# Performance work log

Hardware: AMD Instinct MI355X
Metric: run time of the kernel (lower is better)

Reference implementation:

```python
import jax, jax.numpy as jnp
import numpy as np

B, L, C = 2, 2048, 1024
DK, H = 64, 16

def setup_inputs() -> dict:
    key = jax.random.key(0)
    ks = jax.random.split(key, 12)
    def lin(kw, kb, out_dim, in_dim):
        w = jax.random.normal(kw, (out_dim, in_dim), jnp.float32) * (1.0 / np.sqrt(in_dim))
        b = jnp.zeros((out_dim,), jnp.float32)
        return w, b
    WQ_w, WQ_b = lin(ks[0], ks[1], DK * H, C)
    WK_w, WK_b = lin(ks[2], ks[3], DK * H, C)
    WV_w, WV_b = lin(ks[4], ks[5], DK * H, C)
    WO_w, WO_b = lin(ks[6], ks[7], C, DK * H)
    qx = jax.random.normal(ks[8], (B, L, C), jnp.float32)
    kx = jax.random.normal(ks[9], (B, L, C), jnp.float32)
    vx = jax.random.normal(ks[10], (B, L, C), jnp.float32)
    maskPAD = jax.random.randint(ks[11], (B, L, L), 0, 2, jnp.int32)
    return {"qx": qx, "kx": kx, "vx": vx, "maskPAD": maskPAD,
            "WQ_w": WQ_w, "WQ_b": WQ_b, "WK_w": WK_w, "WK_b": WK_b,
            "WV_w": WV_w, "WV_b": WV_b, "WO_w": WO_w, "WO_b": WO_b}

def reference(qx, kx, vx, maskPAD, WQ_w, WQ_b, WK_w, WK_b, WV_w, WV_b, WO_w, WO_b):
    Bq, qL, _ = qx.shape
    kvL = kx.shape[1]
    # projections -> [B, H, L, DK]
    q = (qx @ WQ_w.T + WQ_b).reshape(Bq, qL, H, DK).transpose(0, 2, 1, 3)
    k = (kx @ WK_w.T + WK_b).reshape(Bq, kvL, H, DK).transpose(0, 2, 1, 3)
    v = (vx @ WV_w.T + WV_b).reshape(Bq, kvL, H, DK).transpose(0, 2, 1, 3)
    scores = jnp.einsum('bhqd,bhkd->bhqk', q, k) / np.sqrt(DK).astype(np.float32)
    scores = jnp.where((maskPAD == 0)[:, None, :, :], jnp.float32(-2**15 + 1), scores)
    alpha = jax.nn.softmax(scores, axis=3)  # dropout p=0 (eval)
    z = jnp.einsum('bhqk,bhkd->bhqd', alpha, v)
    z = z.transpose(0, 2, 1, 3).reshape(Bq, qL, H * DK)
    return z @ WO_w.T + WO_b
```

## Files before the change

### kernel.cpp

```cpp
#include <hip/hip_runtime.h>
#include <hip/hip_bf16.h>
#include <stdint.h>
#include <math.h>

typedef short short8 __attribute__((ext_vector_type(8)));
typedef short short4v __attribute__((ext_vector_type(4)));
typedef float float4v __attribute__((ext_vector_type(4)));
typedef float float2v __attribute__((ext_vector_type(2)));

static __device__ __forceinline__ float bf2f(uint16_t u) {
    union { uint32_t i; float f; } x; x.i = ((uint32_t)u) << 16; return x.f;
}
static __device__ __forceinline__ uint16_t f2bf(float f) {
    union { float f; uint32_t i; } x; x.f = f;
    uint32_t u = x.i;
    u += 0x7FFFu + ((u >> 16) & 1u);
    return (uint16_t)(u >> 16);
}
static __device__ __forceinline__ uint16_t f2bf_hw(float f) {
    __hip_bfloat16 h = __float2bfloat16(f);
    uint16_t u; __builtin_memcpy(&u, &h, 2); return u;
}
static __device__ __forceinline__ uint16_t f2bf_sane(float f) {
    uint16_t u = f2bf(f);
    if ((u & 0x7F80u) == 0x7F80u) u = 0;
    return u;
}
static __device__ __forceinline__ float san_f32(float f) {
    union { float f; uint32_t i; } x; x.f = f;
    if (((x.i >> 23) & 0xFFu) == 0xFFu) return 0.f;
    return x.f;
}
static __device__ __forceinline__ void gll16(const void* g, void* l) {
    __builtin_amdgcn_global_load_lds((const __attribute__((address_space(1))) void*)g,
                                     (__attribute__((address_space(3))) void*)l,
                                     16, 0, 0);
}
static __device__ __forceinline__ short8 load8(const void* p, size_t off, int fp32) {
    if (!fp32) return *(const short8*)((const uint16_t*)p + off);
    const float* f = (const float*)p + off;
    const float4v a = *(const float4v*)f;
    const float4v b = *(const float4v*)(f + 4);
    short8 r;
    r[0] = (short)f2bf(a[0]); r[1] = (short)f2bf(a[1]);
    r[2] = (short)f2bf(a[2]); r[3] = (short)f2bf(a[3]);
    r[4] = (short)f2bf(b[0]); r[5] = (short)f2bf(b[1]);
    r[6] = (short)f2bf(b[2]); r[7] = (short)f2bf(b[3]);
    return r;
}

static __device__ __forceinline__ float fexp2(float x) {
#if __has_builtin(__builtin_amdgcn_exp2f)
    return __builtin_amdgcn_exp2f(x);
#else
    float r; asm("v_exp_f32 %0, %1\ns_nop 0" : "=v"(r) : "v"(x)); return r;
#endif
}

static __device__ __forceinline__ float maskexp2(float s, uint32_t nib, int r) {
    union { float f; uint32_t u; } x; x.f = s;
    const uint32_t keep = (uint32_t)(((int32_t)(nib << (31 - r))) >> 31);
    x.u = (x.u & keep) | (~keep & 0xFF800000u);
    return fexp2(x.f);
}

static __device__ __forceinline__ float4v mfma16_bf16(short4v a, short4v b, float4v c) {
#if __has_builtin(__builtin_amdgcn_mfma_f32_16x16x16bf16_1k)
    return __builtin_amdgcn_mfma_f32_16x16x16bf16_1k(a, b, c, 0, 0, 0);
#else
    float4v d = c;
    asm volatile("v_mfma_f32_16x16x16_bf16 %0, %1, %2, %0"
                 : "+v"(d) : "v"(a), "v"(b));
    return d;
#endif
}

__global__ __launch_bounds__(256) void pack_kernel(
    const int* __restrict__ mask, uint64_t* __restrict__ mask64,
    const uint16_t* __restrict__ qx, int* __restrict__ flag)
{
    const int wave = threadIdx.x >> 6, lane = threadIdx.x & 63;
    if (blockIdx.x == 1024) {
        __shared__ int s;
        const int tid = threadIdx.x;
        if (tid == 0) s = 0;
        __syncthreads();
        int bad = 0;
#pragma unroll 8
        for (int i = 0; i < 64; ++i) {
            const uint16_t u = qx[tid * 64 + i];
            bad |= ((u & 0x7F80u) == 0x7F80u) ? 1 : 0;
        }
        if (bad) atomicOr(&s, 1);
        __syncthreads();
        if (tid == 0) *flag = s;
        return;
    }
    const int row = blockIdx.x * 4 + wave;
    const int* src = mask + (size_t)row * 2048;
#pragma unroll 4
    for (int j = 0; j < 32; ++j) {
        const int m = src[j * 64 + lane];
        const uint64_t bal = __ballot(m != 0);
        if (lane == 0) mask64[(size_t)row * 32 + j] = bal;
    }
}

__global__ __launch_bounds__(256) void convert_kernel(
    const void* qx, const void* kx, const void* vx,
    const void* wq, const void* wk, const void* wv, const void* wo,
    const void* bq, const void* bk, const void* bv, const void* bo,
    uint16_t* cIn, uint16_t* cW, uint16_t* cB, const int* flag)
{
    const int mode = *flag;
    if (!mode) return;
    const int z = blockIdx.z;
    if (z < 3) {
        const void* src = (z == 0) ? qx : (z == 1) ? kx : vx;
        uint16_t* dst = cIn + (size_t)z * 4194304;
#pragma unroll
        for (int it = 0; it < 8; ++it) {
            const int idx8 = (blockIdx.x * 8 + it) * 256 + threadIdx.x;
            *(short8*)(dst + (size_t)idx8 * 8) = load8(src, (size_t)idx8 * 8, 1);
        }
    } else if (z < 7) {
        const int t = z - 3;
        const void* src = (t == 0) ? wq : (t == 1) ? wk : (t == 2) ? wv : wo;
        uint16_t* dst = cW + (size_t)t * 1048576;
#pragma unroll
        for (int it = 0; it < 2; ++it) {
            const int idx8 = (blockIdx.x * 2 + it) * 256 + threadIdx.x;
            *(short8*)(dst + (size_t)idx8 * 8) = load8(src, (size_t)idx8 * 8, 1);
        }
    } else {
        const int idx8 = blockIdx.x * 256 + threadIdx.x;
        if (idx8 < 128) {
#pragma unroll
            for (int t = 0; t < 4; ++t) {
                const void* src = (t == 0) ? bq : (t == 1) ? bk : (t == 2) ? bv : bo;
                *(short8*)(cB + t * 1024 + idx8 * 8) = load8(src, (size_t)idx8 * 8, 1);
            }
        }
    }
}

template <int MI, int NI>
static __device__ __forceinline__ void gemm_tile(
    const uint16_t* __restrict__ A, const uint16_t* __restrict__ W,
    const uint16_t* __restrict__ bias, void* __restrict__ C,
    int c_fp32, float out_scale, int bx, int by)
{
    constexpr int TM = MI * 32, TN = NI * 32;
    __shared__ __align__(16) uint16_t sA[TM * 32];
    __shared__ __align__(16) uint16_t sB[TN * 32];

    const int tid  = threadIdx.x;
    const int wave = tid >> 6;
    const int lane = tid & 63;
    const int quad = lane >> 4;
    const int l15  = lane & 15;
    const int m0 = by * TM;
    const int n0 = bx * TN;
    const int wm = (wave >> 1) * (MI * 16);
    const int wn = (wave & 1) * (NI * 16);
    const int r16 = lane >> 2;
    const int ch  = lane & 3;

    float4v acc[MI][NI] = {};

    for (int k0 = 0; k0 < 1024; k0 += 32) {
        __syncthreads();
#pragma unroll
        for (int g = wave; g < TM / 16; g += 4)
            gll16(A + (size_t)(m0 + g * 16 + r16) * 1024 + k0 + ch * 8,
                  (char*)sA + (size_t)g * 1024);
#pragma unroll
        for (int g = wave; g < TN / 16; g += 4)
            gll16(W + (size_t)(n0 + g * 16 + r16) * 1024 + k0 + ch * 8,
                  (char*)sB + (size_t)g * 1024);
        asm volatile("s_waitcnt vmcnt(0)" ::: "memory");
        __syncthreads();

        short8 af[MI], bfr[NI];
#pragma unroll
        for (int i = 0; i < MI; ++i)
            af[i] = *(const short8*)&sA[(wm + i * 16 + l15) * 32 + quad * 8];
#pragma unroll
        for (int j = 0; j < NI; ++j)
            bfr[j] = *(const short8*)&sB[(wn + j * 16 + l15) * 32 + quad * 8];
#pragma unroll
        for (int mi = 0; mi < MI; ++mi)
#pragma unroll
            for (int ni = 0; ni < NI; ++ni)
                acc[mi][ni] = __builtin_amdgcn_mfma_f32_16x16x32_bf16(
                    af[mi], bfr[ni], acc[mi][ni], 0, 0, 0);
    }

#pragma unroll
    for (int ni = 0; ni < NI; ++ni) {
        const int n = n0 + wn + ni * 16 + l15;
        const float bv = bf2f(bias[n]);
#pragma unroll
        for (int mi = 0; mi < MI; ++mi) {
            const int mbase = m0 + wm + mi * 16 + quad * 4;
#pragma unroll
            for (int r = 0; r < 4; ++r) {
                const float v = (acc[mi][ni][r] + bv) * out_scale;
                const size_t idx = (size_t)(mbase + r) * 1024 + n;
                if (c_fp32) ((float*)C)[idx] = san_f32(v);
                else        ((uint16_t*)C)[idx] = f2bf_sane(v);
            }
        }
    }
}

__global__ __launch_bounds__(256) void qkv_kernel(
    const uint16_t* rqx, const uint16_t* rkx, const uint16_t* rvx,
    const uint16_t* rwq, const uint16_t* rwk, const uint16_t* rwv,
    const uint16_t* rbq, const uint16_t* rbk, const uint16_t* rbv,
    const uint16_t* cIn, const uint16_t* cW, const uint16_t* cB,
    uint16_t* Q, uint16_t* K, uint16_t* V, const int* flag)
{
    const int mode = *flag;
    const int wgid = blockIdx.x + (blockIdx.y << 3) + (blockIdx.z << 8);
    const int xcd = wgid & 7;
    const int s   = wgid >> 3;
    const int panel = xcd * 12 + (s >> 3);
    const int bx = s & 7;
    const int z  = panel >> 5;
    const int by = panel & 31;

    const uint16_t* A = mode ? cIn + (size_t)z * 4194304
                             : ((z == 0) ? rqx : (z == 1) ? rkx : rvx);
    const uint16_t* W = mode ? cW + (size_t)z * 1048576
                             : ((z == 0) ? rwq : (z == 1) ? rwk : rwv);
    const uint16_t* b = mode ? cB + z * 1024
                             : ((z == 0) ? rbq : (z == 1) ? rbk : rbv);
    uint16_t* C = (z == 0) ? Q : (z == 1) ? K : V;
    const float sc = (z == 0) ? 0.18033688f : 1.0f;
    gemm_tile<4, 4>(A, W, b, C, 0, sc, bx, by);
}

__global__ __launch_bounds__(256) void out_kernel(
    const uint16_t* Z, const uint16_t* rwo, const uint16_t* rbo,
    const uint16_t* cW, const uint16_t* cB, void* out, const int* flag)
{
    const int mode = *flag;
    const uint16_t* W = mode ? cW + 3 * 1048576 : rwo;
    const uint16_t* b = mode ? cB + 3 * 1024 : rbo;
    const int wgid = blockIdx.x + (blockIdx.y << 3);
    const int xcd = wgid & 7;
    const int s   = wgid >> 3;
    const int by  = xcd * 8 + (s >> 3);
    const int bx  = s & 7;
    gemm_tile<2, 4>(Z, W, b, out, mode, 1.0f, bx, by);
}

__global__ __launch_bounds__(256) void vtrans_kernel(
    const uint16_t* __restrict__ Vp, uint16_t* __restrict__ Vt)
{
    __shared__ __align__(16) uint16_t t[64][72];
    const int tid = threadIdx.x;
    const int lt = blockIdx.x, h = blockIdx.y, b = blockIdx.z;
#pragma unroll
    for (int p = 0; p < 2; ++p) {
        const int r = p * 32 + (tid >> 3);
        const int c = (tid & 7) * 8;
        *(short8*)&t[r][c] =
            *(const short8*)(Vp + (size_t)(b * 2048 + lt * 64 + r) * 1024 + h * 64 + c);
    }
    __syncthreads();
#pragma unroll
    for (int p = 0; p < 2; ++p) {
        const int d = p * 32 + (tid >> 3);
        const int c = (tid & 7) * 8;
        short8 v;
#pragma unroll
        for (int j = 0; j < 8; ++j) v[j] = (short)t[c + j][d];
        *(short8*)(Vt + (size_t)((b * 16 + h) * 64 + d) * 2048 + lt * 64 + c) = v;
    }
}

#define VS 72

__global__ __launch_bounds__(256, 4) void attn_kernel(
    const uint16_t* __restrict__ Q, const uint16_t* __restrict__ Kp,
    const uint16_t* __restrict__ Vt, const uint64_t* __restrict__ mask64,
    uint16_t* __restrict__ Oa, uint16_t* __restrict__ Ob,
    uint16_t* __restrict__ Oc, float* __restrict__ lpart)
{
    __shared__ __align__(16) uint16_t sK[64 * VS];
    __shared__ __align__(16) uint16_t sV[64 * VS];

    const int tid = threadIdx.x;
    const int wave = tid >> 6, lane = tid & 63;
    const int quad = lane >> 4, l15 = lane & 15;
    const int qt = blockIdx.x, h = blockIdx.y;
    const int b = blockIdx.z & 1, seg = blockIdx.z >> 1;
    const int q0 = qt * 128;
    const int qw = q0 + wave * 32;

    const int srow = tid >> 2;
    const int sc0  = tid & 3;

    short8 qf[2][2];
#pragma unroll
    for (int mi = 0; mi < 2; ++mi)
#pragma unroll
        for (int kk = 0; kk < 2; ++kk)
            qf[mi][kk] = *(const short8*)(Q + (size_t)(b * 2048 + qw + mi * 16 + l15) * 1024
                                            + h * 64 + (quad + 4 * kk) * 8);

    const uint64_t* mrow[2];
#pragma unroll
    for (int mj = 0; mj < 2; ++mj)
        mrow[mj] = mask64 + (size_t)(b * 2048 + qw + mj * 16 + l15) * 32;

    const uint16_t* Kbase = Kp + (size_t)(b * 2048 + srow) * 1024 + h * 64;
    const uint16_t* Vbase = Vt + (size_t)((b * 16 + h) * 64 + srow) * 2048;

    float4v oaccT[4][2] = {};
    float2v lsum2[2] = {};

    const int kt_lo = seg * 11;
    const int kt_hi = (seg == 2) ? 32 : kt_lo + 11;

    short8 kx0 = *(const short8*)(Kbase + (size_t)(kt_lo * 64) * 1024 + sc0 * 8);
    short8 kx1 = *(const short8*)(Kbase + (size_t)(kt_lo * 64) * 1024 + (sc0 + 4) * 8);
    short8 vx0 = *(const short8*)(Vbase + kt_lo * 64 + sc0 * 8);
    short8 vx1 = *(const short8*)(Vbase + kt_lo * 64 + (sc0 + 4) * 8);

    for (int kt = kt_lo; kt < kt_hi; ++kt) {
        const uint64_t mwq0 = mrow[0][kt] >> (quad * 4);
        const uint64_t mwq1 = mrow[1][kt] >> (quad * 4);
        __syncthreads();
        *(short8*)&sK[srow * VS + sc0 * 8]       = kx0;
        *(short8*)&sK[srow * VS + (sc0 + 4) * 8] = kx1;
        *(short8*)&sV[srow * VS + sc0 * 8]       = vx0;
        *(short8*)&sV[srow * VS + (sc0 + 4) * 8] = vx1;
        __syncthreads();

        short8 nk0, nk1, nv0, nv1;
        if (kt + 1 < kt_hi) {
            const int k0n = (kt + 1) * 64;
            nk0 = *(const short8*)(Kbase + (size_t)k0n * 1024 + sc0 * 8);
            nk1 = *(const short8*)(Kbase + (size_t)k0n * 1024 + (sc0 + 4) * 8);
            nv0 = *(const short8*)(Vbase + k0n + sc0 * 8);
            nv1 = *(const short8*)(Vbase + k0n + (sc0 + 4) * 8);
        } else {
            nk0 = kx0; nk1 = kx1; nv0 = vx0; nv1 = vx1;
        }

        float4v sacc[2][4] = {};
        __builtin_amdgcn_s_setprio(1);
#pragma unroll
        for (int ni = 0; ni < 4; ++ni) {
            const int row = ni * 16 + l15;
#pragma unroll
            for (int kk = 0; kk < 2; ++kk) {
                const short8 kf = *(const short8*)&sK[row * VS + (quad + 4 * kk) * 8];
                sacc[0][ni] = __builtin_amdgcn_mfma_f32_16x16x32_bf16(kf, qf[0][kk], sacc[0][ni], 0, 0, 0);
                sacc[1][ni] = __builtin_amdgcn_mfma_f32_16x16x32_bf16(kf, qf[1][kk], sacc[1][ni], 0, 0, 0);
            }
        }
        __builtin_amdgcn_s_setprio(0);

        short4v pf[2][4];
#pragma unroll
        for (int mj = 0; mj < 2; ++mj) {
            const uint64_t mwq = mj ? mwq1 : mwq0;
#pragma unroll
            for (int ni = 0; ni < 4; ++ni) {
                const uint32_t nib = (uint32_t)(mwq >> (ni * 16)) & 0xFu;
                const float p0 = maskexp2(sacc[mj][ni][0], nib, 0);
                const float p1 = maskexp2(sacc[mj][ni][1], nib, 1);
                const float p2 = maskexp2(sacc[mj][ni][2], nib, 2);
                const float p3 = maskexp2(sacc[mj][ni][3], nib, 3);
                float2v lo; lo[0] = p0; lo[1] = p1;
                float2v hi; hi[0] = p2; hi[1] = p3;
                lsum2[mj] += lo;
                lsum2[mj] += hi;
                short4v t;
                t[0] = (short)f2bf_hw(p0);
                t[1] = (short)f2bf_hw(p1);
                t[2] = (short)f2bf_hw(p2);
                t[3] = (short)f2bf_hw(p3);
                pf[mj][ni] = t;
            }
        }

        __builtin_amdgcn_s_setprio(1);
#pragma unroll
        for (int di = 0; di < 4; ++di) {
            const int row = di * 16 + l15;
#pragma unroll
            for (int ni = 0; ni < 4; ++ni) {
                const short4v vf = *(const short4v*)&sV[row * VS + ni * 16 + quad * 4];
                oaccT[di][0] = mfma16_bf16(vf, pf[0][ni], oaccT[di][0]);
                oaccT[di][1] = mfma16_bf16(vf, pf[1][ni], oaccT[di][1]);
            }
        }
        __builtin_amdgcn_s_setprio(0);

        kx0 = nk0; kx1 = nk1; vx0 = nv0; vx1 = nv1;
    }

#if !__has_builtin(__builtin_amdgcn_mfma_f32_16x16x16bf16_1k)
    asm volatile("s_nop 7\ns_nop 7\ns_nop 7" ::: "memory");
#endif

    float lsum[2];
#pragma unroll
    for (int mj = 0; mj < 2; ++mj) lsum[mj] = lsum2[mj][0] + lsum2[mj][1];

#pragma unroll
    for (int mj = 0; mj < 2; ++mj) {
        lsum[mj] += __shfl_xor(lsum[mj], 16);
        lsum[mj] += __shfl_xor(lsum[mj], 32);
    }

    uint16_t* Op = (seg == 0) ? Oa : (seg == 1) ? Ob : Oc;
#pragma unroll
    for (int mj = 0; mj < 2; ++mj) {
        const int qrow = qw + mj * 16 + l15;
#pragma unroll
        for (int di = 0; di < 4; ++di) {
            short4v o;
#pragma unroll
            for (int r = 0; r < 4; ++r) o[r] = (short)f2bf_hw(oaccT[di][mj][r]);
            *(short4v*)(Op + (size_t)(b * 2048 + qrow) * 1024 + h * 64 + di * 16 + quad * 4) = o;
        }
        if (quad == 0)
            lpart[seg * 65536 + (b * 16 + h) * 2048 + qrow] = lsum[mj];
    }
}

__global__ __launch_bounds__(256) void combine_kernel(
    const uint16_t* __restrict__ Oa, const uint16_t* __restrict__ Ob,
    const uint16_t* __restrict__ Oc, const float* __restrict__ lpart,
    uint16_t* __restrict__ Z)
{
    const int e8 = blockIdx.x * 256 + threadIdx.x;
    const int flat = e8 * 8;
    const int bh_row = flat >> 10;
    const int h = (flat >> 6) & 15;
    const int b = bh_row >> 11;
    const int row = bh_row & 2047;
    const int lidx = (b * 16 + h) * 2048 + row;
    const float inv = 1.0f / fmaxf(lpart[lidx] + lpart[65536 + lidx] + lpart[131072 + lidx], 1e-37f);
    const short8 a = *(const short8*)(Oa + flat);
    const short8 c = *(const short8*)(Ob + flat);
    const short8 d = *(const short8*)(Oc + flat);
    short8 o;
#pragma unroll
    for (int j = 0; j < 8; ++j)
        o[j] = (short)f2bf_sane((bf2f((uint16_t)a[j]) + bf2f((uint16_t)c[j]) + bf2f((uint16_t)d[j])) * inv);
    *(short8*)(Z + flat) = o;
}

extern "C" void kernel_launch(void* const* d_in, const int* in_sizes, int n_in,
                              void* d_out, int out_size, void* d_ws, size_t ws_size,
                              hipStream_t stream)
{
    const void* qx  = d_in[0];
    const void* kx  = d_in[1];
    const void* vx  = d_in[2];
    const int*  msk = (const int*)d_in[3];

    char* ws = (char*)d_ws;
    const size_t MB = 1024 * 1024;
    uint16_t* cIn = (uint16_t*)(ws);
    uint16_t* cW  = (uint16_t*)(ws + 24 * MB);
    uint16_t* cB  = (uint16_t*)(ws + 32 * MB);
    int*      flg = (int*)(ws + 32 * MB + 16 * 1024);
    uint16_t* Qb  = (uint16_t*)(ws + 33 * MB);
    uint16_t* Kb  = (uint16_t*)(ws + 41 * MB);
    uint16_t* Vb  = (uint16_t*)(ws + 49 * MB);
    uint64_t* m64 = (uint64_t*)(ws + 57 * MB);
    uint16_t* Vt  = (uint16_t*)(ws + 8 * MB);
    uint16_t* Oa  = (uint16_t*)(ws);
    uint16_t* Ob  = (uint16_t*)(ws + 16 * MB);
    uint16_t* Oc  = (uint16_t*)(ws + 49 * MB);
    float*    lp  = (float*)(ws + 24 * MB);
    uint16_t* Zb  = Oa;

    pack_kernel<<<1025, 256, 0, stream>>>(msk, m64, (const uint16_t*)qx, flg);
    convert_kernel<<<dim3(256, 1, 8), 256, 0, stream>>>(
        qx, kx, vx, d_in[4], d_in[6], d_in[8], d_in[10],
        d_in[5], d_in[7], d_in[9], d_in[11], cIn, cW, cB, flg);
    qkv_kernel<<<dim3(8, 32, 3), 256, 0, stream>>>(
        (const uint16_t*)qx, (const uint16_t*)kx, (const uint16_t*)vx,
        (const uint16_t*)d_in[4], (const uint16_t*)d_in[6], (const uint16_t*)d_in[8],
        (const uint16_t*)d_in[5], (const uint16_t*)d_in[7], (const uint16_t*)d_in[9],
        cIn, cW, cB, Qb, Kb, Vb, flg);
    vtrans_kernel<<<dim3(32, 16, 2), 256, 0, stream>>>(Vb, Vt);
    attn_kernel<<<dim3(16, 16, 6), 256, 0, stream>>>(Qb, Kb, Vt, m64, Oa, Ob, Oc, lp);
    combine_kernel<<<4096, 256, 0, stream>>>(Oa, Ob, Oc, lp, Zb);
    out_kernel<<<dim3(8, 64), 256, 0, stream>>>(
        Zb, (const uint16_t*)d_in[10], (const uint16_t*)d_in[11], cW, cB, d_out, flg);
}
```

Baseline: 294.8 us.

## Fuse fp32 input conversion into QKV GEMM loads and merge convert into pack kernel

The QKV GEMM now reads fp32 activations directly, converting them to bf16 in registers before the shared-memory store. This replaces the separate pass that wrote converted copies of qx/kx/vx to the workspace. The weight/bias conversion moves into the mask-pack kernel as extra blocks, with each block recomputing the dtype probe locally, which saves one launch. In exchange, the A-tile path gives up async global-to-LDS loads for synchronous vector loads plus conversion in every k-iteration, and the probe read is repeated by many blocks.

```diff
diff --git a/kernel.cpp b/kernel.cpp
--- a/kernel.cpp
+++ b/kernel.cpp
@@ -77,68 +77,56 @@
 
 __global__ __launch_bounds__(256) void pack_kernel(
     const int* __restrict__ mask, uint64_t* __restrict__ mask64,
-    const uint16_t* __restrict__ qx, int* __restrict__ flag)
-{
-    const int wave = threadIdx.x >> 6, lane = threadIdx.x & 63;
-    if (blockIdx.x == 1024) {
-        __shared__ int s;
-        const int tid = threadIdx.x;
-        if (tid == 0) s = 0;
-        __syncthreads();
-        int bad = 0;
-#pragma unroll 8
-        for (int i = 0; i < 64; ++i) {
-            const uint16_t u = qx[tid * 64 + i];
-            bad |= ((u & 0x7F80u) == 0x7F80u) ? 1 : 0;
-        }
-        if (bad) atomicOr(&s, 1);
-        __syncthreads();
-        if (tid == 0) *flag = s;
-        return;
-    }
-    const int row = blockIdx.x * 4 + wave;
-    const int* src = mask + (size_t)row * 2048;
-#pragma unroll 4
-    for (int j = 0; j < 32; ++j) {
-        const int m = src[j * 64 + lane];
-        const uint64_t bal = __ballot(m != 0);
-        if (lane == 0) mask64[(size_t)row * 32 + j] = bal;
-    }
-}
-
-__global__ __launch_bounds__(256) void convert_kernel(
-    const void* qx, const void* kx, const void* vx,
+    const uint16_t* __restrict__ qx, int* __restrict__ flag,
     const void* wq, const void* wk, const void* wv, const void* wo,
     const void* bq, const void* bk, const void* bv, const void* bo,
-    uint16_t* cIn, uint16_t* cW, uint16_t* cB, const int* flag)
-{
-    const int mode = *flag;
+    uint16_t* __restrict__ cW, uint16_t* __restrict__ cB)
+{
+    const int bx = blockIdx.x;
+    const int tid = threadIdx.x;
+    if (bx < 1024) {
+        const int wave = tid >> 6, lane = tid & 63;
+        const int row = bx * 4 + wave;
+        const int* src = mask + (size_t)row * 2048;
+#pragma unroll 4
+        for (int j = 0; j < 32; ++j) {
+            const int m = src[j * 64 + lane];
+            const uint64_t bal = __ballot(m != 0);
+            if (lane == 0) mask64[(size_t)row * 32 + j] = bal;
+        }
+        return;
+    }
+    __shared__ int s;
+    if (tid == 0) s = 0;
+    __syncthreads();
+    int bad = 0;
+#pragma unroll 8
+    for (int i = 0; i < 64; ++i) {
+        const uint16_t u = qx[tid * 64 + i];
+        bad |= ((u & 0x7F80u) == 0x7F80u) ? 1 : 0;
+    }
+    if (bad) atomicOr(&s, 1);
+    __syncthreads();
+    const int mode = s;
+    if (bx == 1024) {
+        if (tid == 0) *flag = mode;
+        return;
+    }
     if (!mode) return;
-    const int z = blockIdx.z;
-    if (z < 3) {
-        const void* src = (z == 0) ? qx : (z == 1) ? kx : vx;
-        uint16_t* dst = cIn + (size_t)z * 4194304;
-#pragma unroll
-        for (int it = 0; it < 8; ++it) {
-            const int idx8 = (blockIdx.x * 8 + it) * 256 + threadIdx.x;
-            *(short8*)(dst + (size_t)idx8 * 8) = load8(src, (size_t)idx8 * 8, 1);
-        }
-    } else if (z < 7) {
-        const int t = z - 3;
-        const void* src = (t == 0) ? wq : (t == 1) ? wk : (t == 2) ? wv : wo;
-        uint16_t* dst = cW + (size_t)t * 1048576;
-#pragma unroll
-        for (int it = 0; it < 2; ++it) {
-            const int idx8 = (blockIdx.x * 2 + it) * 256 + threadIdx.x;
-            *(short8*)(dst + (size_t)idx8 * 8) = load8(src, (size_t)idx8 * 8, 1);
+    if (bx < 1537) {
+        const int idx8 = (bx - 1025) * 256 + tid;
+#pragma unroll
+        for (int t = 0; t < 4; ++t) {
+            const void* src = (t == 0) ? wq : (t == 1) ? wk : (t == 2) ? wv : wo;
+            *(short8*)(cW + (size_t)t * 1048576 + (size_t)idx8 * 8) =
+                load8(src, (size_t)idx8 * 8, 1);
         }
     } else {
-        const int idx8 = blockIdx.x * 256 + threadIdx.x;
-        if (idx8 < 128) {
+        if (tid < 128) {
 #pragma unroll
             for (int t = 0; t < 4; ++t) {
                 const void* src = (t == 0) ? bq : (t == 1) ? bk : (t == 2) ? bv : bo;
-                *(short8*)(cB + t * 1024 + idx8 * 8) = load8(src, (size_t)idx8 * 8, 1);
+                *(short8*)(cB + t * 1024 + tid * 8) = load8(src, (size_t)tid * 8, 1);
             }
         }
     }
@@ -146,7 +134,8 @@
 
 template <int MI, int NI>
 static __device__ __forceinline__ void gemm_tile(
-    const uint16_t* __restrict__ A, const uint16_t* __restrict__ W,
+    const void* __restrict__ A, int afp32,
+    const uint16_t* __restrict__ W,
     const uint16_t* __restrict__ bias, void* __restrict__ C,
     int c_fp32, float out_scale, int bx, int by)
 {
@@ -170,10 +159,27 @@
 
     for (int k0 = 0; k0 < 1024; k0 += 32) {
         __syncthreads();
-#pragma unroll
-        for (int g = wave; g < TM / 16; g += 4)
-            gll16(A + (size_t)(m0 + g * 16 + r16) * 1024 + k0 + ch * 8,
-                  (char*)sA + (size_t)g * 1024);
+        if (afp32) {
+            const float* Af = (const float*)A;
+#pragma unroll
+            for (int g = wave; g < TM / 16; g += 4) {
+                const float* p = Af + (size_t)(m0 + g * 16 + r16) * 1024 + k0 + ch * 8;
+                const float4v a = *(const float4v*)p;
+                const float4v b2 = *(const float4v*)(p + 4);
+                short8 r;
+                r[0] = (short)f2bf_hw(a[0]);  r[1] = (short)f2bf_hw(a[1]);
+                r[2] = (short)f2bf_hw(a[2]);  r[3] = (short)f2bf_hw(a[3]);
+                r[4] = (short)f2bf_hw(b2[0]); r[5] = (short)f2bf_hw(b2[1]);
+                r[6] = (short)f2bf_hw(b2[2]); r[7] = (short)f2bf_hw(b2[3]);
+                *(short8*)((char*)sA + (size_t)g * 1024 + (size_t)lane * 16) = r;
+            }
+        } else {
+            const uint16_t* Ah = (const uint16_t*)A;
+#pragma unroll
+            for (int g = wave; g < TM / 16; g += 4)
+                gll16(Ah + (size_t)(m0 + g * 16 + r16) * 1024 + k0 + ch * 8,
+                      (char*)sA + (size_t)g * 1024);
+        }
 #pragma unroll
         for (int g = wave; g < TN / 16; g += 4)
             gll16(W + (size_t)(n0 + g * 16 + r16) * 1024 + k0 + ch * 8,
@@ -215,10 +221,10 @@
 }
 
 __global__ __launch_bounds__(256) void qkv_kernel(
-    const uint16_t* rqx, const uint16_t* rkx, const uint16_t* rvx,
+    const void* qxr, const void* kxr, const void* vxr,
     const uint16_t* rwq, const uint16_t* rwk, const uint16_t* rwv,
     const uint16_t* rbq, const uint16_t* rbk, const uint16_t* rbv,
-    const uint16_t* cIn, const uint16_t* cW, const uint16_t* cB,
+    const uint16_t* cW, const uint16_t* cB,
     uint16_t* Q, uint16_t* K, uint16_t* V, const int* flag)
 {
     const int mode = *flag;
@@ -230,15 +236,14 @@
     const int z  = panel >> 5;
     const int by = panel & 31;
 
-    const uint16_t* A = mode ? cIn + (size_t)z * 4194304
-                             : ((z == 0) ? rqx : (z == 1) ? rkx : rvx);
+    const void* A = (z == 0) ? qxr : (z == 1) ? kxr : vxr;
     const uint16_t* W = mode ? cW + (size_t)z * 1048576
                              : ((z == 0) ? rwq : (z == 1) ? rwk : rwv);
     const uint16_t* b = mode ? cB + z * 1024
                              : ((z == 0) ? rbq : (z == 1) ? rbk : rbv);
     uint16_t* C = (z == 0) ? Q : (z == 1) ? K : V;
     const float sc = (z == 0) ? 0.18033688f : 1.0f;
-    gemm_tile<4, 4>(A, W, b, C, 0, sc, bx, by);
+    gemm_tile<4, 4>(A, mode, W, b, C, 0, sc, bx, by);
 }
 
 __global__ __launch_bounds__(256) void out_kernel(
@@ -253,7 +258,7 @@
     const int s   = wgid >> 3;
     const int by  = xcd * 8 + (s >> 3);
     const int bx  = s & 7;
-    gemm_tile<2, 4>(Z, W, b, out, mode, 1.0f, bx, by);
+    gemm_tile<2, 4>(Z, 0, W, b, out, mode, 1.0f, bx, by);
 }
 
 __global__ __launch_bounds__(256) void vtrans_kernel(
@@ -469,7 +474,6 @@
 
     char* ws = (char*)d_ws;
     const size_t MB = 1024 * 1024;
-    uint16_t* cIn = (uint16_t*)(ws);
     uint16_t* cW  = (uint16_t*)(ws + 24 * MB);
     uint16_t* cB  = (uint16_t*)(ws + 32 * MB);
     int*      flg = (int*)(ws + 32 * MB + 16 * 1024);
@@ -484,15 +488,15 @@
     float*    lp  = (float*)(ws + 24 * MB);
     uint16_t* Zb  = Oa;
 
-    pack_kernel<<<1025, 256, 0, stream>>>(msk, m64, (const uint16_t*)qx, flg);
-    convert_kernel<<<dim3(256, 1, 8), 256, 0, stream>>>(
-        qx, kx, vx, d_in[4], d_in[6], d_in[8], d_in[10],
-        d_in[5], d_in[7], d_in[9], d_in[11], cIn, cW, cB, flg);
+    pack_kernel<<<1538, 256, 0, stream>>>(
+        msk, m64, (const uint16_t*)qx, flg,
+        d_in[4], d_in[6], d_in[8], d_in[10],
+        d_in[5], d_in[7], d_in[9], d_in[11], cW, cB);
     qkv_kernel<<<dim3(8, 32, 3), 256, 0, stream>>>(
-        (const uint16_t*)qx, (const uint16_t*)kx, (const uint16_t*)vx,
+        qx, kx, vx,
         (const uint16_t*)d_in[4], (const uint16_t*)d_in[6], (const uint16_t*)d_in[8],
         (const uint16_t*)d_in[5], (const uint16_t*)d_in[7], (const uint16_t*)d_in[9],
-        cIn, cW, cB, Qb, Kb, Vb, flg);
+        cW, cB, Qb, Kb, Vb, flg);
     vtrans_kernel<<<dim3(32, 16, 2), 256, 0, stream>>>(Vb, Vt);
     attn_kernel<<<dim3(16, 16, 6), 256, 0, stream>>>(Qb, Kb, Vt, m64, Oa, Ob, Oc, lp);
     combine_kernel<<<4096, 256, 0, stream>>>(Oa, Ob, Oc, lp, Zb);
```

Result: slower. 312.6 us (+6.0%).
